# Performance work log

Measured on AMD Instinct MI355X. Metric: run time of the kernel, lower is better.

The kernel has to match this reference:

```python
import jax, jax.numpy as jnp
import numpy as np

B, S, D, H = 2, 2048, 1024, 16
DH = D // H


def setup_inputs() -> dict:
    key = jax.random.key(0)
    ks = jax.random.split(key, 12)
    f = lambda k, sh: jax.random.normal(k, sh, dtype=jnp.float32)
    inp = {"q": f(ks[0], (B, S, D)), "k": f(ks[1], (B, S, D)), "v": f(ks[2], (B, S, D))}
    scale = 1.0 / np.sqrt(D)
    names = ["q", "k", "v", "o"]
    for i, n in enumerate(names):
        inp["W" + n] = f(ks[3 + i], (D, D)) * scale
        inp["b" + n] = f(ks[7 + i], (D,)) * scale
    # causal mask: True = masked out
    inp["mask"] = jnp.triu(jnp.ones((S, S), dtype=bool), k=1)[None, None]
    return inp


def _rope(x):
    # x: [b, h, s, dh]; non-standard RoPE from AbsPositionEncoding
    s, dh = x.shape[2], x.shape[3]
    inv = jnp.exp(jnp.arange(0, dh, 2, dtype=jnp.float32) * (-(4.0 * jnp.log(jnp.float32(10.0))) / dh))
    pos = jnp.arange(s, dtype=jnp.float32)[:, None]
    sin = jnp.sin(pos * inv)  # [s, dh/2]
    cos = jnp.cos(pos * inv)
    x1 = x[..., 0::2]
    x2 = x[..., 1::2]
    out = jnp.stack([x1 * sin - x2 * cos, -x1 * cos - x2 * sin], axis=-1)
    return out.reshape(x.shape)


def reference(q, k, v, Wq, bq, Wk, bk, Wv, bv, Wo, bo, mask):
    b, s, d = q.shape
    h, dh = H, DH

    def proj(x, W, bias):
        return (x @ W.T + bias).reshape(b, -1, h, dh).transpose(0, 2, 1, 3)

    Q = proj(q, Wq, bq)
    K = proj(k, Wk, bk)
    V = proj(v, Wv, bv)
    PQ = _rope(Q)
    PK = _rope(K)
    # NOTE: source's forward() path applies NO 1/sqrt(dh) scaling
    scores = jnp.einsum('bhqd,bhkd->bhqk', PQ, PK)
    neg = jnp.finfo(scores.dtype).min
    scores = jnp.where(mask, neg, scores)
    p = jax.nn.softmax(scores, axis=-1)
    p = jnp.where(mask, jnp.float32(0.0), p)
    out = jnp.einsum('bhqk,bhkd->bhqd', p, V)
    out = out.transpose(0, 2, 1, 3).reshape(b, s, d)
    return out @ Wo.T + bo
```

## Files before the change

kernel.cpp:

```cpp
#include <hip/hip_runtime.h>
#include <stdint.h>

#define BB 2
#define SS 2048
#define DD 1024
#define HH 16
#define DH 64
#define MM 4096

typedef __attribute__((ext_vector_type(8))) short short8;
typedef __attribute__((ext_vector_type(4))) float floatx4;
typedef __attribute__((ext_vector_type(16))) float floatx16;
typedef unsigned short u16;

#define MFMA16(a,b,c) __builtin_amdgcn_mfma_f32_16x16x32_bf16((a),(b),(c),0,0,0)
#define MFMA32(a,b,c) __builtin_amdgcn_mfma_f32_32x32x16_bf16((a),(b),(c),0,0,0)

__device__ __forceinline__ u16 f2bf(float f) {
  unsigned u = __float_as_uint(f);
  u += 0x7fffu + ((u >> 16) & 1u);
  return (u16)(u >> 16);
}

__device__ __forceinline__ unsigned cvtpk(float lo, float hi2) {
  unsigned r;
  asm("v_cvt_pk_bf16_f32 %0, %1, %2" : "=v"(r) : "v"(lo), "v"(hi2));
  return r;
}

__device__ __forceinline__ void gll16(const void* g, void* l) {
  __builtin_amdgcn_global_load_lds((const __attribute__((address_space(1))) void*)g,
                                   (__attribute__((address_space(3))) void*)l,
                                   16, 0, 0);
}

__global__ __launch_bounds__(256) void sincos_k(float2* __restrict__ tab) {
  const int t = blockIdx.x * 256 + threadIdx.x;
  const int s = t >> 5, j = t & 31;
  const float inv = expf(-(float)j * (0.125f * 2.302585092994046f));
  const float a = (float)s * inv;
  tab[t] = make_float2(sinf(a), cosf(a));
}

__global__ __launch_bounds__(256) void conv_qkv(const float* __restrict__ a, const float* __restrict__ b,
                                                const float* __restrict__ c,
                                                u16* __restrict__ oa, u16* __restrict__ ob, u16* __restrict__ oc) {
  const float* s = blockIdx.y == 0 ? a : (blockIdx.y == 1 ? b : c);
  u16* d = blockIdx.y == 0 ? oa : (blockIdx.y == 1 ? ob : oc);
  const int i = (blockIdx.x * 256 + threadIdx.x) * 4;
  const float4 x = *(const float4*)(s + i);
  ushort4 p; p.x = f2bf(x.x); p.y = f2bf(x.y); p.z = f2bf(x.z); p.w = f2bf(x.w);
  *(ushort4*)(d + i) = p;
}

__global__ __launch_bounds__(256) void conv_w(const float* __restrict__ a, const float* __restrict__ b,
                                              const float* __restrict__ c, const float* __restrict__ d4,
                                              u16* __restrict__ oa, u16* __restrict__ ob,
                                              u16* __restrict__ oc, u16* __restrict__ od) {
  const float* s = blockIdx.y == 0 ? a : (blockIdx.y == 1 ? b : (blockIdx.y == 2 ? c : d4));
  u16* d = blockIdx.y == 0 ? oa : (blockIdx.y == 1 ? ob : (blockIdx.y == 2 ? oc : od));
  const int i = (blockIdx.x * 256 + threadIdx.x) * 4;
  const float4 x = *(const float4*)(s + i);
  ushort4 p; p.x = f2bf(x.x); p.y = f2bf(x.y); p.z = f2bf(x.z); p.w = f2bf(x.w);
  *(ushort4*)(d + i) = p;
}

__device__ __forceinline__ void gemm_core64(const u16* __restrict__ A, const u16* __restrict__ Bt,
                                            int K, u16* As, u16* Bs, floatx4 acc[2][4],
                                            int m0, int n0) {
  const int tid = threadIdx.x;
  const int w = tid >> 6, l = tid & 63;
  const int lr = l & 15, lq = l >> 4;
  const int wm = (w >> 1) * 32, wn = (w & 1) * 64;

#pragma unroll
  for (int i = 0; i < 2; ++i)
#pragma unroll
    for (int j = 0; j < 4; ++j) acc[i][j] = (floatx4){0.f, 0.f, 0.f, 0.f};

  const int arow = w * 16 + (l >> 2);
  const int brow = w * 32 + (l >> 2);
  const int scol = (l & 3) * 8;
  const u16* ag = A + (size_t)(m0 + arow) * K + scol;
  const u16* bg = Bt + (size_t)(n0 + brow) * K + scol;
  u16* as0 = &As[w * 512];
  u16* bs0 = &Bs[w * 1024];

  for (int k0 = 0; k0 < K; k0 += 32) {
    gll16(ag + k0, as0);
    gll16(bg + k0, bs0);
    gll16(bg + (size_t)16 * K + k0, bs0 + 512);
    __syncthreads();
    short8 af[2], bfv[4];
#pragma unroll
    for (int i = 0; i < 2; ++i) af[i] = *(const short8*)&As[(wm + i * 16 + lr) * 32 + lq * 8];
#pragma unroll
    for (int j = 0; j < 4; ++j) bfv[j] = *(const short8*)&Bs[(wn + j * 16 + lr) * 32 + lq * 8];
    __builtin_amdgcn_s_setprio(1);
#pragma unroll
    for (int i = 0; i < 2; ++i)
#pragma unroll
      for (int j = 0; j < 4; ++j) acc[i][j] = MFMA16(af[i], bfv[j], acc[i][j]);
    __builtin_amdgcn_s_setprio(0);
    __syncthreads();
  }
}

__global__ __launch_bounds__(256) void gemm3_fused(
    const u16* __restrict__ A0, const u16* __restrict__ A1, const u16* __restrict__ A2,
    const u16* __restrict__ B0, const u16* __restrict__ B1, const u16* __restrict__ B2,
    const float* __restrict__ c0, const float* __restrict__ c1, const float* __restrict__ c2,
    u16* __restrict__ Qro, u16* __restrict__ Kro, u16* __restrict__ Vtr,
    const float2* __restrict__ tab) {
  __shared__ alignas(16) u16 As[64 * 32];
  __shared__ alignas(16) u16 Bs[128 * 32];
  const int z = blockIdx.z;
  const u16* A = z == 0 ? A0 : (z == 1 ? A1 : A2);
  const u16* Bt = z == 0 ? B0 : (z == 1 ? B1 : B2);
  const float* bias = z == 0 ? c0 : (z == 1 ? c1 : c2);
  const int m0 = blockIdx.y * 64, n0 = blockIdx.x * 128;

  floatx4 acc[2][4];
  gemm_core64(A, Bt, DD, As, Bs, acc, m0, n0);

  const int tid = threadIdx.x;
  const int w = tid >> 6, l = tid & 63;
  const int lr = l & 15, lq = l >> 4;
  const int wm = (w >> 1) * 32, wn = (w & 1) * 64;

  if (z == 2) {
#pragma unroll
    for (int i = 0; i < 2; ++i) {
      const int row = m0 + wm + i * 16 + lq * 4;
      const int b = row >> 11, s = row & (SS - 1);
#pragma unroll
      for (int j = 0; j < 4; ++j) {
        const int col = n0 + wn + j * 16 + lr;
        const int h = col >> 6, e = col & 63;
        const float bv = bias[col];
        ushort4 pk;
        pk.x = f2bf(acc[i][j][0] + bv);
        pk.y = f2bf(acc[i][j][1] + bv);
        pk.z = f2bf(acc[i][j][2] + bv);
        pk.w = f2bf(acc[i][j][3] + bv);
        *(ushort4*)(Vtr + ((size_t)(b * HH + h) * DH + e) * SS + s) = pk;
      }
    }
  } else {
    u16* dst = z ? Kro : Qro;
#pragma unroll
    for (int i = 0; i < 2; ++i) {
#pragma unroll
      for (int j = 0; j < 4; ++j) {
        const int col = n0 + wn + j * 16 + lr;
        const int h = col >> 6, e = col & 63;
        const float bv = bias[col];
#pragma unroll
        for (int r = 0; r < 4; ++r) {
          const int row = m0 + wm + i * 16 + lq * 4 + r;
          const int b = row >> 11, s = row & (SS - 1);
          const float v = acc[i][j][r] + bv;
          const float p = __shfl_xor(v, 1);
          const float2 sc = tab[s * 32 + (e >> 1)];
          const float ov = ((e & 1) == 0) ? (v * sc.x - p * sc.y)
                                          : (-p * sc.y - v * sc.x);
          dst[((size_t)(b * HH + h) * SS + s) * DH + e] = f2bf(ov);
        }
      }
    }
  }
}

__global__ __launch_bounds__(256) void gemm_bt(const u16* __restrict__ A, const u16* __restrict__ Bt,
                                               const float* __restrict__ bias, float* __restrict__ C,
                                               int M, int N, int K) {
  __shared__ alignas(16) u16 As[64 * 32];
  __shared__ alignas(16) u16 Bs[128 * 32];
  const int m0 = blockIdx.y * 64, n0 = blockIdx.x * 128;
  floatx4 acc[2][4];
  gemm_core64(A, Bt, K, As, Bs, acc, m0, n0);

  const int tid = threadIdx.x;
  const int w = tid >> 6, l = tid & 63;
  const int lr = l & 15, lq = l >> 4;
  const int wm = (w >> 1) * 32, wn = (w & 1) * 64;
#pragma unroll
  for (int i = 0; i < 2; ++i) {
    const int row = m0 + wm + i * 16 + lq * 4;
#pragma unroll
    for (int j = 0; j < 4; ++j) {
      const int col = n0 + wn + j * 16 + lr;
      const float bv = bias[col];
      float* cp = C + (size_t)row * N + col;
#pragma unroll
      for (int r = 0; r < 4; ++r) cp[(size_t)r * N] = acc[i][j][r] + bv;
    }
  }
}

__global__ __launch_bounds__(128) void attn_fwd(const u16* __restrict__ Qr, const u16* __restrict__ Kr,
                                                const u16* __restrict__ Vt, u16* __restrict__ O) {
  __shared__ alignas(16) u16 Ks[2][64 * 64];
  __shared__ alignas(16) u16 Vs[2][64 * 64];
  const int bid = blockIdx.x;
  const int qt = 31 - (bid >> 5);
  const int bh = bid & 31;
  const int w = threadIdx.x >> 6, l = threadIdx.x & 63;
  const int ql = l & 31, hi = l >> 5;
  const int qw0 = qt * 64 + w * 32;
  const u16* Qh = Qr + (size_t)bh * SS * DH;
  const u16* Kh = Kr + (size_t)bh * SS * DH;
  const u16* Vh = Vt + (size_t)bh * DH * SS;

  short8 qf[4];
#pragma unroll
  for (int i = 0; i < 4; ++i)
    qf[i] = *(const short8*)(Qh + (size_t)(qw0 + ql) * DH + i * 16 + hi * 8);

  floatx16 oacc[2];
#pragma unroll
  for (int dt = 0; dt < 2; ++dt)
#pragma unroll
    for (int r = 0; r < 16; ++r) oacc[dt][r] = 0.f;
  float mrun = -1e30f, lrun = 0.f;

  const int srow = w * 32 + (l >> 3);
  const int sgofs = ((((l & 7) * 16) ^ (((l >> 3) & 7) << 4)) >> 1);
  const int swzb = (ql & 7) << 4;

#define STAGE(buf, kv0)                                                                    \
  do {                                                                                     \
    gll16(Kh + (size_t)((kv0) + srow) * DH + sgofs,        &Ks[buf][(w * 32) * 64]);       \
    gll16(Kh + (size_t)((kv0) + srow + 8) * DH + sgofs,    &Ks[buf][(w * 32 + 8) * 64]);   \
    gll16(Kh + (size_t)((kv0) + srow + 16) * DH + sgofs,   &Ks[buf][(w * 32 + 16) * 64]);  \
    gll16(Kh + (size_t)((kv0) + srow + 24) * DH + sgofs,   &Ks[buf][(w * 32 + 24) * 64]);  \
    gll16(Vh + (size_t)srow * SS + (kv0) + sgofs,          &Vs[buf][(w * 32) * 64]);       \
    gll16(Vh + (size_t)(srow + 8) * SS + (kv0) + sgofs,    &Vs[buf][(w * 32 + 8) * 64]);   \
    gll16(Vh + (size_t)(srow + 16) * SS + (kv0) + sgofs,   &Vs[buf][(w * 32 + 16) * 64]);  \
    gll16(Vh + (size_t)(srow + 24) * SS + (kv0) + sgofs,   &Vs[buf][(w * 32 + 24) * 64]);  \
  } while (0)

  const int T = qt + 1;
  STAGE(0, 0);
  __syncthreads();

  for (int t = 0; t < T; ++t) {
    const int cur = t & 1;
    if (t < T - 1) STAGE(cur ^ 1, (t + 1) * 64);
    const int kv0 = t * 64;

    floatx16 st[2];
#pragma unroll
    for (int tt = 0; tt < 2; ++tt)
#pragma unroll
      for (int r = 0; r < 16; ++r) st[tt][r] = 0.f;
    __builtin_amdgcn_s_setprio(1);
#pragma unroll
    for (int tt = 0; tt < 2; ++tt)
#pragma unroll
      for (int i = 0; i < 4; ++i) {
        const u16* kp = &Ks[cur][(tt * 32 + ql) * 64 + (((32 * i + 16 * hi) ^ swzb) >> 1)];
        st[tt] = MFMA32(*(const short8*)kp, qf[i], st[tt]);
      }
    __builtin_amdgcn_s_setprio(0);

    if (t == T - 1) {
#pragma unroll
      for (int tt = 0; tt < 2; ++tt)
#pragma unroll
        for (int r = 0; r < 16; ++r) {
          const int kv = kv0 + tt * 32 + (r & 3) + 8 * (r >> 2) + 4 * hi;
          if (kv > qw0 + ql) st[tt][r] = -1e30f;
        }
    }

    floatx16 mx;
#pragma unroll
    for (int r = 0; r < 16; ++r) mx[r] = fmaxf(st[0][r], st[1][r]);
    float m8[8];
#pragma unroll
    for (int r = 0; r < 8; ++r) m8[r] = fmaxf(mx[r], mx[r + 8]);
    float m4a = fmaxf(m8[0], m8[4]), m4b = fmaxf(m8[1], m8[5]);
    float m4c = fmaxf(m8[2], m8[6]), m4d = fmaxf(m8[3], m8[7]);
    float tmax = fmaxf(fmaxf(m4a, m4b), fmaxf(m4c, m4d));
    tmax = fmaxf(tmax, __shfl_xor(tmax, 32));

    const float mn = fmaxf(mrun, tmax);
    const float sc = __expf(mrun - mn);
    mrun = mn;
    float ps = 0.f;
#pragma unroll
    for (int tt = 0; tt < 2; ++tt)
#pragma unroll
      for (int r = 0; r < 16; ++r) {
        const float p = __expf(st[tt][r] - mn);
        st[tt][r] = p;
        ps += p;
      }
    ps += __shfl_xor(ps, 32);
    lrun = lrun * sc + ps;
#pragma unroll
    for (int dt = 0; dt < 2; ++dt)
#pragma unroll
      for (int r = 0; r < 16; ++r) oacc[dt][r] *= sc;

    short8 pfrag[4];
#pragma unroll
    for (int c = 0; c < 4; ++c) {
      const int tt = c >> 1;
      const int A0r = 2 * (c & 1), A1r = A0r + 1;
      const unsigned P00 = cvtpk(st[tt][4 * A0r + 0], st[tt][4 * A0r + 1]);
      const unsigned P01 = cvtpk(st[tt][4 * A0r + 2], st[tt][4 * A0r + 3]);
      const unsigned P10 = cvtpk(st[tt][4 * A1r + 0], st[tt][4 * A1r + 1]);
      const unsigned P11 = cvtpk(st[tt][4 * A1r + 2], st[tt][4 * A1r + 3]);
      const unsigned S0 = hi ? P00 : P10;
      const unsigned S1 = hi ? P01 : P11;
      const unsigned R0 = (unsigned)__shfl_xor((int)S0, 32);
      const unsigned R1 = (unsigned)__shfl_xor((int)S1, 32);
      union { unsigned u[4]; short8 s; } fd;
      fd.u[0] = hi ? R0 : P00;
      fd.u[1] = hi ? R1 : P01;
      fd.u[2] = hi ? P10 : R0;
      fd.u[3] = hi ? P11 : R1;
      pfrag[c] = fd.s;
    }

    __builtin_amdgcn_s_setprio(1);
#pragma unroll
    for (int dt = 0; dt < 2; ++dt)
#pragma unroll
      for (int c = 0; c < 4; ++c) {
        const u16* vp = &Vs[cur][(dt * 32 + ql) * 64 + (((32 * c + 16 * hi) ^ swzb) >> 1)];
        oacc[dt] = MFMA32(*(const short8*)vp, pfrag[c], oacc[dt]);
      }
    __builtin_amdgcn_s_setprio(0);
    __syncthreads();
  }
#undef STAGE

  const float inv = 1.0f / lrun;
  const int b = bh >> 4, h = bh & 15;
  u16* orow = O + ((size_t)(b * SS + qw0 + ql)) * DD + h * DH;
#pragma unroll
  for (int dt = 0; dt < 2; ++dt)
#pragma unroll
    for (int g = 0; g < 4; ++g) {
      ushort4 pk;
      pk.x = f2bf(oacc[dt][4 * g + 0] * inv);
      pk.y = f2bf(oacc[dt][4 * g + 1] * inv);
      pk.z = f2bf(oacc[dt][4 * g + 2] * inv);
      pk.w = f2bf(oacc[dt][4 * g + 3] * inv);
      *(ushort4*)(orow + dt * 32 + 8 * g + 4 * hi) = pk;
    }
}

extern "C" void kernel_launch(void* const* d_in, const int* in_sizes, int n_in,
                              void* d_out, int out_size, void* d_ws, size_t ws_size,
                              hipStream_t stream) {
  (void)in_sizes; (void)n_in; (void)out_size; (void)ws_size;
  const float* q  = (const float*)d_in[0];
  const float* k  = (const float*)d_in[1];
  const float* v  = (const float*)d_in[2];
  const float* Wq = (const float*)d_in[3];
  const float* bq = (const float*)d_in[4];
  const float* Wk = (const float*)d_in[5];
  const float* bk = (const float*)d_in[6];
  const float* Wv = (const float*)d_in[7];
  const float* bv = (const float*)d_in[8];
  const float* Wo = (const float*)d_in[9];
  const float* bo = (const float*)d_in[10];
  float* out = (float*)d_out;

  char* ws = (char*)d_ws;
  size_t off = 0;
  auto carve = [&](size_t bytes) { char* p = ws + off; off += (bytes + 255) & ~(size_t)255; return p; };
  u16* qb   = (u16*)carve((size_t)MM * DD * 2);
  u16* kb   = (u16*)carve((size_t)MM * DD * 2);
  u16* vb   = (u16*)carve((size_t)MM * DD * 2);
  u16* wqb  = (u16*)carve((size_t)DD * DD * 2);
  u16* wkb  = (u16*)carve((size_t)DD * DD * 2);
  u16* wvb  = (u16*)carve((size_t)DD * DD * 2);
  u16* wob  = (u16*)carve((size_t)DD * DD * 2);
  u16* Qro  = (u16*)carve((size_t)MM * DD * 2);
  u16* Kro  = (u16*)carve((size_t)MM * DD * 2);
  u16* Vtr  = (u16*)carve((size_t)MM * DD * 2);
  float2* tab = (float2*)carve((size_t)SS * 32 * 8);
  u16* Ob = qb;

  sincos_k<<<SS * 32 / 256, 256, 0, stream>>>(tab);
  conv_qkv<<<dim3(MM * DD / 1024, 3), 256, 0, stream>>>(q, k, v, qb, kb, vb);
  conv_w<<<dim3(DD * DD / 1024, 4), 256, 0, stream>>>(Wq, Wk, Wv, Wo, wqb, wkb, wvb, wob);
  gemm3_fused<<<dim3(DD / 128, MM / 64, 3), 256, 0, stream>>>(qb, kb, vb, wqb, wkb, wvb,
                                                              bq, bk, bv, Qro, Kro, Vtr, tab);
  attn_fwd<<<32 * BB * HH, 128, 0, stream>>>(Qro, Kro, Vtr, Ob);
  gemm_bt<<<dim3(DD / 128, MM / 64), 256, 0, stream>>>(Ob, wob, bo, out, MM, DD, DD);
}
```

Measured before the change: 269.1 us.

## Merge prep kernels, enlarge QKV GEMM tiles, use 128-query attention blocks

Measured after the change: 264.0 us. About the same (-1.9%).

```diff
diff --git a/kernel.cpp b/kernel.cpp
--- a/kernel.cpp
+++ b/kernel.cpp
@@ -34,35 +34,83 @@
                                    16, 0, 0);
 }
 
-__global__ __launch_bounds__(256) void sincos_k(float2* __restrict__ tab) {
-  const int t = blockIdx.x * 256 + threadIdx.x;
-  const int s = t >> 5, j = t & 31;
-  const float inv = expf(-(float)j * (0.125f * 2.302585092994046f));
-  const float a = (float)s * inv;
-  tab[t] = make_float2(sinf(a), cosf(a));
-}
-
-__global__ __launch_bounds__(256) void conv_qkv(const float* __restrict__ a, const float* __restrict__ b,
-                                                const float* __restrict__ c,
-                                                u16* __restrict__ oa, u16* __restrict__ ob, u16* __restrict__ oc) {
-  const float* s = blockIdx.y == 0 ? a : (blockIdx.y == 1 ? b : c);
-  u16* d = blockIdx.y == 0 ? oa : (blockIdx.y == 1 ? ob : oc);
-  const int i = (blockIdx.x * 256 + threadIdx.x) * 4;
-  const float4 x = *(const float4*)(s + i);
-  ushort4 p; p.x = f2bf(x.x); p.y = f2bf(x.y); p.z = f2bf(x.z); p.w = f2bf(x.w);
-  *(ushort4*)(d + i) = p;
-}
-
-__global__ __launch_bounds__(256) void conv_w(const float* __restrict__ a, const float* __restrict__ b,
-                                              const float* __restrict__ c, const float* __restrict__ d4,
-                                              u16* __restrict__ oa, u16* __restrict__ ob,
-                                              u16* __restrict__ oc, u16* __restrict__ od) {
-  const float* s = blockIdx.y == 0 ? a : (blockIdx.y == 1 ? b : (blockIdx.y == 2 ? c : d4));
-  u16* d = blockIdx.y == 0 ? oa : (blockIdx.y == 1 ? ob : (blockIdx.y == 2 ? oc : od));
-  const int i = (blockIdx.x * 256 + threadIdx.x) * 4;
-  const float4 x = *(const float4*)(s + i);
-  ushort4 p; p.x = f2bf(x.x); p.y = f2bf(x.y); p.z = f2bf(x.z); p.w = f2bf(x.w);
-  *(ushort4*)(d + i) = p;
+__global__ __launch_bounds__(256) void prep(
+    const float* __restrict__ q, const float* __restrict__ k, const float* __restrict__ v,
+    const float* __restrict__ Wq, const float* __restrict__ Wk,
+    const float* __restrict__ Wv, const float* __restrict__ Wo,
+    u16* __restrict__ qb, u16* __restrict__ kb, u16* __restrict__ vb,
+    u16* __restrict__ wqb, u16* __restrict__ wkb, u16* __restrict__ wvb, u16* __restrict__ wob,
+    float2* __restrict__ tab) {
+  int bid = blockIdx.x;
+  if (bid < 256) {
+    const int t = bid * 256 + threadIdx.x;
+    const int s = t >> 5, j = t & 31;
+    const float inv = expf(-(float)j * (0.125f * 2.302585092994046f));
+    const float a = (float)s * inv;
+    tab[t] = make_float2(sinf(a), cosf(a));
+    return;
+  }
+  bid -= 256;
+  const float* src;
+  u16* dst;
+  int x;
+  if (bid < 12288) {
+    const int z = bid >> 12;
+    x = bid & 4095;
+    src = z == 0 ? q : (z == 1 ? k : v);
+    dst = z == 0 ? qb : (z == 1 ? kb : vb);
+  } else {
+    bid -= 12288;
+    const int z = bid >> 10;
+    x = bid & 1023;
+    src = z == 0 ? Wq : (z == 1 ? Wk : (z == 2 ? Wv : Wo));
+    dst = z == 0 ? wqb : (z == 1 ? wkb : (z == 2 ? wvb : wob));
+  }
+  const int i = (x * 256 + threadIdx.x) * 4;
+  const float4 xv = *(const float4*)(src + i);
+  ushort4 p; p.x = f2bf(xv.x); p.y = f2bf(xv.y); p.z = f2bf(xv.z); p.w = f2bf(xv.w);
+  *(ushort4*)(dst + i) = p;
+}
+
+__device__ __forceinline__ void gemm_core128(const u16* __restrict__ A, const u16* __restrict__ Bt,
+                                             int K, u16* As, u16* Bs, floatx4 acc[4][4],
+                                             int m0, int n0) {
+  const int tid = threadIdx.x;
+  const int w = tid >> 6, l = tid & 63;
+  const int lr = l & 15, lq = l >> 4;
+  const int wm = (w >> 1) * 64, wn = (w & 1) * 64;
+
+#pragma unroll
+  for (int i = 0; i < 4; ++i)
+#pragma unroll
+    for (int j = 0; j < 4; ++j) acc[i][j] = (floatx4){0.f, 0.f, 0.f, 0.f};
+
+  const int srow = w * 32 + (l >> 2);
+  const int scol = (l & 3) * 8;
+  const u16* ag = A + (size_t)(m0 + srow) * K + scol;
+  const u16* bg = Bt + (size_t)(n0 + srow) * K + scol;
+  u16* as0 = &As[w * 1024];
+  u16* bs0 = &Bs[w * 1024];
+
+  for (int k0 = 0; k0 < K; k0 += 32) {
+    gll16(ag + k0, as0);
+    gll16(ag + (size_t)16 * K + k0, as0 + 512);
+    gll16(bg + k0, bs0);
+    gll16(bg + (size_t)16 * K + k0, bs0 + 512);
+    __syncthreads();
+    short8 af[4], bfv[4];
+#pragma unroll
+    for (int i = 0; i < 4; ++i) af[i] = *(const short8*)&As[(wm + i * 16 + lr) * 32 + lq * 8];
+#pragma unroll
+    for (int j = 0; j < 4; ++j) bfv[j] = *(const short8*)&Bs[(wn + j * 16 + lr) * 32 + lq * 8];
+    __builtin_amdgcn_s_setprio(1);
+#pragma unroll
+    for (int i = 0; i < 4; ++i)
+#pragma unroll
+      for (int j = 0; j < 4; ++j) acc[i][j] = MFMA16(af[i], bfv[j], acc[i][j]);
+    __builtin_amdgcn_s_setprio(0);
+    __syncthreads();
+  }
 }
 
 __device__ __forceinline__ void gemm_core64(const u16* __restrict__ A, const u16* __restrict__ Bt,
@@ -112,25 +160,25 @@
     const float* __restrict__ c0, const float* __restrict__ c1, const float* __restrict__ c2,
     u16* __restrict__ Qro, u16* __restrict__ Kro, u16* __restrict__ Vtr,
     const float2* __restrict__ tab) {
-  __shared__ alignas(16) u16 As[64 * 32];
+  __shared__ alignas(16) u16 As[128 * 32];
   __shared__ alignas(16) u16 Bs[128 * 32];
   const int z = blockIdx.z;
   const u16* A = z == 0 ? A0 : (z == 1 ? A1 : A2);
   const u16* Bt = z == 0 ? B0 : (z == 1 ? B1 : B2);
   const float* bias = z == 0 ? c0 : (z == 1 ? c1 : c2);
-  const int m0 = blockIdx.y * 64, n0 = blockIdx.x * 128;
-
-  floatx4 acc[2][4];
-  gemm_core64(A, Bt, DD, As, Bs, acc, m0, n0);
+  const int m0 = blockIdx.y * 128, n0 = blockIdx.x * 128;
+
+  floatx4 acc[4][4];
+  gemm_core128(A, Bt, DD, As, Bs, acc, m0, n0);
 
   const int tid = threadIdx.x;
   const int w = tid >> 6, l = tid & 63;
   const int lr = l & 15, lq = l >> 4;
-  const int wm = (w >> 1) * 32, wn = (w & 1) * 64;
+  const int wm = (w >> 1) * 64, wn = (w & 1) * 64;
 
   if (z == 2) {
 #pragma unroll
-    for (int i = 0; i < 2; ++i) {
+    for (int i = 0; i < 4; ++i) {
       const int row = m0 + wm + i * 16 + lq * 4;
       const int b = row >> 11, s = row & (SS - 1);
 #pragma unroll
@@ -149,7 +197,7 @@
   } else {
     u16* dst = z ? Kro : Qro;
 #pragma unroll
-    for (int i = 0; i < 2; ++i) {
+    for (int i = 0; i < 4; ++i) {
 #pragma unroll
       for (int j = 0; j < 4; ++j) {
         const int col = n0 + wn + j * 16 + lr;
@@ -198,16 +246,16 @@
   }
 }
 
-__global__ __launch_bounds__(128) void attn_fwd(const u16* __restrict__ Qr, const u16* __restrict__ Kr,
+__global__ __launch_bounds__(256) void attn_fwd(const u16* __restrict__ Qr, const u16* __restrict__ Kr,
                                                 const u16* __restrict__ Vt, u16* __restrict__ O) {
   __shared__ alignas(16) u16 Ks[2][64 * 64];
   __shared__ alignas(16) u16 Vs[2][64 * 64];
   const int bid = blockIdx.x;
-  const int qt = 31 - (bid >> 5);
+  const int qt = 15 - (bid >> 5);
   const int bh = bid & 31;
   const int w = threadIdx.x >> 6, l = threadIdx.x & 63;
   const int ql = l & 31, hi = l >> 5;
-  const int qw0 = qt * 64 + w * 32;
+  const int qw0 = qt * 128 + w * 32;
   const u16* Qh = Qr + (size_t)bh * SS * DH;
   const u16* Kh = Kr + (size_t)bh * SS * DH;
   const u16* Vh = Vt + (size_t)bh * DH * SS;
@@ -224,23 +272,19 @@
     for (int r = 0; r < 16; ++r) oacc[dt][r] = 0.f;
   float mrun = -1e30f, lrun = 0.f;
 
-  const int srow = w * 32 + (l >> 3);
+  const int srow = w * 16 + (l >> 3);
   const int sgofs = ((((l & 7) * 16) ^ (((l >> 3) & 7) << 4)) >> 1);
   const int swzb = (ql & 7) << 4;
 
-#define STAGE(buf, kv0)                                                                    \
-  do {                                                                                     \
-    gll16(Kh + (size_t)((kv0) + srow) * DH + sgofs,        &Ks[buf][(w * 32) * 64]);       \
-    gll16(Kh + (size_t)((kv0) + srow + 8) * DH + sgofs,    &Ks[buf][(w * 32 + 8) * 64]);   \
-    gll16(Kh + (size_t)((kv0) + srow + 16) * DH + sgofs,   &Ks[buf][(w * 32 + 16) * 64]);  \
-    gll16(Kh + (size_t)((kv0) + srow + 24) * DH + sgofs,   &Ks[buf][(w * 32 + 24) * 64]);  \
-    gll16(Vh + (size_t)srow * SS + (kv0) + sgofs,          &Vs[buf][(w * 32) * 64]);       \
-    gll16(Vh + (size_t)(srow + 8) * SS + (kv0) + sgofs,    &Vs[buf][(w * 32 + 8) * 64]);   \
-    gll16(Vh + (size_t)(srow + 16) * SS + (kv0) + sgofs,   &Vs[buf][(w * 32 + 16) * 64]);  \
-    gll16(Vh + (size_t)(srow + 24) * SS + (kv0) + sgofs,   &Vs[buf][(w * 32 + 24) * 64]);  \
+#define STAGE(buf, kv0)                                                                  \
+  do {                                                                                   \
+    gll16(Kh + (size_t)((kv0) + srow) * DH + sgofs,       &Ks[buf][(w * 16) * 64]);      \
+    gll16(Kh + (size_t)((kv0) + srow + 8) * DH + sgofs,   &Ks[buf][(w * 16 + 8) * 64]);  \
+    gll16(Vh + (size_t)srow * SS + (kv0) + sgofs,         &Vs[buf][(w * 16) * 64]);      \
+    gll16(Vh + (size_t)(srow + 8) * SS + (kv0) + sgofs,   &Vs[buf][(w * 16 + 8) * 64]);  \
   } while (0)
 
-  const int T = qt + 1;
+  const int T = 2 * qt + 2;
   STAGE(0, 0);
   __syncthreads();
 
@@ -249,91 +293,93 @@
     if (t < T - 1) STAGE(cur ^ 1, (t + 1) * 64);
     const int kv0 = t * 64;
 
-    floatx16 st[2];
-#pragma unroll
-    for (int tt = 0; tt < 2; ++tt)
-#pragma unroll
-      for (int r = 0; r < 16; ++r) st[tt][r] = 0.f;
-    __builtin_amdgcn_s_setprio(1);
-#pragma unroll
-    for (int tt = 0; tt < 2; ++tt)
-#pragma unroll
-      for (int i = 0; i < 4; ++i) {
-        const u16* kp = &Ks[cur][(tt * 32 + ql) * 64 + (((32 * i + 16 * hi) ^ swzb) >> 1)];
-        st[tt] = MFMA32(*(const short8*)kp, qf[i], st[tt]);
+    if (kv0 <= qw0 + 31) {
+      floatx16 st[2];
+#pragma unroll
+      for (int tt = 0; tt < 2; ++tt)
+#pragma unroll
+        for (int r = 0; r < 16; ++r) st[tt][r] = 0.f;
+      __builtin_amdgcn_s_setprio(1);
+#pragma unroll
+      for (int tt = 0; tt < 2; ++tt)
+#pragma unroll
+        for (int i = 0; i < 4; ++i) {
+          const u16* kp = &Ks[cur][(tt * 32 + ql) * 64 + (((32 * i + 16 * hi) ^ swzb) >> 1)];
+          st[tt] = MFMA32(*(const short8*)kp, qf[i], st[tt]);
+        }
+      __builtin_amdgcn_s_setprio(0);
+
+      if (kv0 + 63 > qw0) {
+#pragma unroll
+        for (int tt = 0; tt < 2; ++tt)
+#pragma unroll
+          for (int r = 0; r < 16; ++r) {
+            const int kv = kv0 + tt * 32 + (r & 3) + 8 * (r >> 2) + 4 * hi;
+            if (kv > qw0 + ql) st[tt][r] = -1e30f;
+          }
       }
-    __builtin_amdgcn_s_setprio(0);
-
-    if (t == T - 1) {
+
+      floatx16 mx;
+#pragma unroll
+      for (int r = 0; r < 16; ++r) mx[r] = fmaxf(st[0][r], st[1][r]);
+      float m8[8];
+#pragma unroll
+      for (int r = 0; r < 8; ++r) m8[r] = fmaxf(mx[r], mx[r + 8]);
+      float m4a = fmaxf(m8[0], m8[4]), m4b = fmaxf(m8[1], m8[5]);
+      float m4c = fmaxf(m8[2], m8[6]), m4d = fmaxf(m8[3], m8[7]);
+      float tmax = fmaxf(fmaxf(m4a, m4b), fmaxf(m4c, m4d));
+      tmax = fmaxf(tmax, __shfl_xor(tmax, 32));
+
+      const float mn = fmaxf(mrun, tmax);
+      const float sc = __expf(mrun - mn);
+      mrun = mn;
+      float ps = 0.f;
 #pragma unroll
       for (int tt = 0; tt < 2; ++tt)
 #pragma unroll
         for (int r = 0; r < 16; ++r) {
-          const int kv = kv0 + tt * 32 + (r & 3) + 8 * (r >> 2) + 4 * hi;
-          if (kv > qw0 + ql) st[tt][r] = -1e30f;
+          const float p = __expf(st[tt][r] - mn);
+          st[tt][r] = p;
+          ps += p;
         }
+      ps += __shfl_xor(ps, 32);
+      lrun = lrun * sc + ps;
+#pragma unroll
+      for (int dt = 0; dt < 2; ++dt)
+#pragma unroll
+        for (int r = 0; r < 16; ++r) oacc[dt][r] *= sc;
+
+      short8 pfrag[4];
+#pragma unroll
+      for (int c = 0; c < 4; ++c) {
+        const int tt = c >> 1;
+        const int A0r = 2 * (c & 1), A1r = A0r + 1;
+        const unsigned P00 = cvtpk(st[tt][4 * A0r + 0], st[tt][4 * A0r + 1]);
+        const unsigned P01 = cvtpk(st[tt][4 * A0r + 2], st[tt][4 * A0r + 3]);
+        const unsigned P10 = cvtpk(st[tt][4 * A1r + 0], st[tt][4 * A1r + 1]);
+        const unsigned P11 = cvtpk(st[tt][4 * A1r + 2], st[tt][4 * A1r + 3]);
+        const unsigned S0 = hi ? P00 : P10;
+        const unsigned S1 = hi ? P01 : P11;
+        const unsigned R0 = (unsigned)__shfl_xor((int)S0, 32);
+        const unsigned R1 = (unsigned)__shfl_xor((int)S1, 32);
+        union { unsigned u[4]; short8 s; } fd;
+        fd.u[0] = hi ? R0 : P00;
+        fd.u[1] = hi ? R1 : P01;
+        fd.u[2] = hi ? P10 : R0;
+        fd.u[3] = hi ? P11 : R1;
+        pfrag[c] = fd.s;
+      }
+
+      __builtin_amdgcn_s_setprio(1);
+#pragma unroll
+      for (int dt = 0; dt < 2; ++dt)
+#pragma unroll
+        for (int c = 0; c < 4; ++c) {
+          const u16* vp = &Vs[cur][(dt * 32 + ql) * 64 + (((32 * c + 16 * hi) ^ swzb) >> 1)];
+          oacc[dt] = MFMA32(*(const short8*)vp, pfrag[c], oacc[dt]);
+        }
+      __builtin_amdgcn_s_setprio(0);
     }
-
-    floatx16 mx;
-#pragma unroll
-    for (int r = 0; r < 16; ++r) mx[r] = fmaxf(st[0][r], st[1][r]);
-    float m8[8];
-#pragma unroll
-    for (int r = 0; r < 8; ++r) m8[r] = fmaxf(mx[r], mx[r + 8]);
-    float m4a = fmaxf(m8[0], m8[4]), m4b = fmaxf(m8[1], m8[5]);
-    float m4c = fmaxf(m8[2], m8[6]), m4d = fmaxf(m8[3], m8[7]);
-    float tmax = fmaxf(fmaxf(m4a, m4b), fmaxf(m4c, m4d));
-    tmax = fmaxf(tmax, __shfl_xor(tmax, 32));
-
-    const float mn = fmaxf(mrun, tmax);
-    const float sc = __expf(mrun - mn);
-    mrun = mn;
-    float ps = 0.f;
-#pragma unroll
-    for (int tt = 0; tt < 2; ++tt)
-#pragma unroll
-      for (int r = 0; r < 16; ++r) {
-        const float p = __expf(st[tt][r] - mn);
-        st[tt][r] = p;
-        ps += p;
-      }
-    ps += __shfl_xor(ps, 32);
-    lrun = lrun * sc + ps;
-#pragma unroll
-    for (int dt = 0; dt < 2; ++dt)
-#pragma unroll
-      for (int r = 0; r < 16; ++r) oacc[dt][r] *= sc;
-
-    short8 pfrag[4];
-#pragma unroll
-    for (int c = 0; c < 4; ++c) {
-      const int tt = c >> 1;
-      const int A0r = 2 * (c & 1), A1r = A0r + 1;
-      const unsigned P00 = cvtpk(st[tt][4 * A0r + 0], st[tt][4 * A0r + 1]);
-      const unsigned P01 = cvtpk(st[tt][4 * A0r + 2], st[tt][4 * A0r + 3]);
-      const unsigned P10 = cvtpk(st[tt][4 * A1r + 0], st[tt][4 * A1r + 1]);
-      const unsigned P11 = cvtpk(st[tt][4 * A1r + 2], st[tt][4 * A1r + 3]);
-      const unsigned S0 = hi ? P00 : P10;
-      const unsigned S1 = hi ? P01 : P11;
-      const unsigned R0 = (unsigned)__shfl_xor((int)S0, 32);
-      const unsigned R1 = (unsigned)__shfl_xor((int)S1, 32);
-      union { unsigned u[4]; short8 s; } fd;
-      fd.u[0] = hi ? R0 : P00;
-      fd.u[1] = hi ? R1 : P01;
-      fd.u[2] = hi ? P10 : R0;
-      fd.u[3] = hi ? P11 : R1;
-      pfrag[c] = fd.s;
-    }
-
-    __builtin_amdgcn_s_setprio(1);
-#pragma unroll
-    for (int dt = 0; dt < 2; ++dt)
-#pragma unroll
-      for (int c = 0; c < 4; ++c) {
-        const u16* vp = &Vs[cur][(dt * 32 + ql) * 64 + (((32 * c + 16 * hi) ^ swzb) >> 1)];
-        oacc[dt] = MFMA32(*(const short8*)vp, pfrag[c], oacc[dt]);
-      }
-    __builtin_amdgcn_s_setprio(0);
     __syncthreads();
   }
 #undef STAGE
@@ -387,11 +433,10 @@
   float2* tab = (float2*)carve((size_t)SS * 32 * 8);
   u16* Ob = qb;
 
-  sincos_k<<<SS * 32 / 256, 256, 0, stream>>>(tab);
-  conv_qkv<<<dim3(MM * DD / 1024, 3), 256, 0, stream>>>(q, k, v, qb, kb, vb);
-  conv_w<<<dim3(DD * DD / 1024, 4), 256, 0, stream>>>(Wq, Wk, Wv, Wo, wqb, wkb, wvb, wob);
-  gemm3_fused<<<dim3(DD / 128, MM / 64, 3), 256, 0, stream>>>(qb, kb, vb, wqb, wkb, wvb,
-                                                              bq, bk, bv, Qro, Kro, Vtr, tab);
-  attn_fwd<<<32 * BB * HH, 128, 0, stream>>>(Qro, Kro, Vtr, Ob);
+  prep<<<256 + 3 * 4096 + 4 * 1024, 256, 0, stream>>>(q, k, v, Wq, Wk, Wv, Wo,
+                                                      qb, kb, vb, wqb, wkb, wvb, wob, tab);
+  gemm3_fused<<<dim3(DD / 128, MM / 128, 3), 256, 0, stream>>>(qb, kb, vb, wqb, wkb, wvb,
+                                                               bq, bk, bv, Qro, Kro, Vtr, tab);
+  attn_fwd<<<16 * BB * HH, 256, 0, stream>>>(Qro, Kro, Vtr, Ob);
   gemm_bt<<<dim3(DD / 128, MM / 64), 256, 0, stream>>>(Ob, wob, bo, out, MM, DD, DD);
 }
```
